# Optimization experiments

Measured on AMD Instinct MI355X. Metric: run time of the kernel, lower is better.

## Reference

```python
import jax, jax.numpy as jnp
import numpy as np

C = 4096
C8 = C // 8  # 512, must equal h*w
B, H, W = 32, 16, 32


def setup_inputs() -> dict:
    key = jax.random.key(0)
    ks = jax.random.split(key, 8)
    s = 0.02
    return {
        "x": jax.random.normal(ks[0], (B, C, H, W), dtype=jnp.float32),
        "Wq": jax.random.normal(ks[1], (C8, C), dtype=jnp.float32) * s,
        "bq": jax.random.normal(ks[2], (C8,), dtype=jnp.float32) * s,
        "Wk": jax.random.normal(ks[3], (C8, C), dtype=jnp.float32) * s,
        "bk": jax.random.normal(ks[4], (C8,), dtype=jnp.float32) * s,
        "Wv": jax.random.normal(ks[5], (C, C), dtype=jnp.float32) * s,
        "bv": jax.random.normal(ks[6], (C,), dtype=jnp.float32) * s,
        "gamma": jax.random.normal(ks[7], (1,), dtype=jnp.float32),
    }


def reference(x, Wq, bq, Wk, bk, Wv, bv, gamma):
    b, c, h, w = x.shape
    xf = x.reshape(b, c, h * w)               # (b, c, hw)
    # 1x1 conv == per-position linear over channels
    q = jnp.einsum("oc,bcl->bol", Wq, xf) + bq[None, :, None]   # (b, c8, hw)
    k = jnp.einsum("oc,bcl->bol", Wk, xf) + bk[None, :, None]   # (b, c8, hw)
    v = jnp.einsum("oc,bcl->bol", Wv, xf) + bv[None, :, None]   # (b, c, hw)
    # energy = bmm(Q, K^T): (b, c8, c8); no sqrt(d) scaling (faithful)
    energy = jnp.einsum("bol,bpl->bop", q, k)
    attn = jax.nn.softmax(energy, axis=-1)
    # out = bmm(V, attn^T): out[b,c,p] = sum_k V[b,c,k] * attn[b,p,k]
    out = jnp.einsum("bck,bpk->bcp", v, attn)  # requires hw == c8
    out = out.reshape(b, c, h, w)
    return gamma * out + x
```

## Files before the change

### kernel.cpp

```cpp
#include <hip/hip_runtime.h>


typedef _Float16 f16;
typedef _Float16 h8 __attribute__((ext_vector_type(8)));
typedef _Float16 h4 __attribute__((ext_vector_type(4)));
typedef float fx4 __attribute__((ext_vector_type(4)));

#define CC  4096
#define C8  512
#define HWD 512
#define NB  32

__device__ __forceinline__ h8 ldfragC(const char* s, int row, int cb) {
  const int b = ((row << 7) | cb) ^ ((row & 7) << 4);
  return *reinterpret_cast<const h8*>(s + b);
}

#define AS1C(p) ((const __attribute__((address_space(1))) unsigned int*)(p))
#define AS3(p)  ((__attribute__((address_space(3))) unsigned int*)(p))


#define STAGE_ALL(bufsel) { \
  char* la_ = smem + ((bufsel) << 16); \
  char* lb_ = la_ + 32768; \
  _Pragma("unroll") for (int q = 0; q < 4; ++q) { \
    __builtin_amdgcn_global_load_lds(AS1C(pA[q]), AS3(la_ + (q << 13) + w1024), 16, 0, 0); \
    __builtin_amdgcn_global_load_lds(AS1C(pB[q]), AS3(lb_ + (q << 13) + w1024), 16, 0, 0); \
    pA[q] += 128; pB[q] += 128; } }

#define STAGE2(bufsel, q) { \
  char* la_ = smem + ((bufsel) << 16); \
  char* lb_ = la_ + 32768; \
  __builtin_amdgcn_global_load_lds(AS1C(pA[q]), AS3(la_ + ((q) << 13) + w1024), 16, 0, 0); \
  __builtin_amdgcn_global_load_lds(AS1C(pB[q]), AS3(lb_ + ((q) << 13) + w1024), 16, 0, 0); \
  pA[q] += 128; pB[q] += 128; }

#define DSREADS_A(dst, hm, kh) \
  _Pragma("unroll") for (int f = 0; f < 4; ++f) \
    dst[f] = ldfragC(At, wr * 128 + (hm) * 64 + f * 16 + frow, (kh) * 64 + kq);

#define DSREADS_B(dst, kh) \
  _Pragma("unroll") for (int g = 0; g < 4; ++g) \
    dst[g] = ldfragC(Bt, wc * 64 + g * 16 + frow, (kh) * 64 + kq);

#define MMA16(hm, av, bv) \
  __builtin_amdgcn_s_setprio(1); \
  _Pragma("unroll") for (int f = 0; f < 4; ++f) \
  _Pragma("unroll") for (int g = 0; g < 4; ++g) \
    acc[(hm) * 4 + f][g] = __builtin_amdgcn_mfma_f32_16x16x32_f16( \
        av[f], bv[g], acc[(hm) * 4 + f][g], 0, 0, 0); \
  __builtin_amdgcn_s_setprio(0);

#define KTILE(cur, DOSTAGE) { \
  const bool dost_ = (DOSTAGE); \
  const char* At = smem + ((cur) << 16); \
  const char* Bt = At + 32768; \
  h8 a0[4], a1[4], b0[4], b1[4]; \
  asm volatile("s_waitcnt vmcnt(0)" ::: "memory"); \
  __builtin_amdgcn_s_barrier(); \
   \
  DSREADS_A(a0, 0, 0) DSREADS_B(b0, 0) \
  if (dost_) { STAGE2((cur) ^ 1, 0) STAGE2((cur) ^ 1, 1) } \
  __builtin_amdgcn_s_barrier(); \
  asm volatile("s_waitcnt lgkmcnt(0)"); \
  MMA16(0, a0, b0) \
  __builtin_amdgcn_s_barrier(); \
   \
  DSREADS_A(a1, 1, 0) \
  if (dost_) { STAGE2((cur) ^ 1, 2) STAGE2((cur) ^ 1, 3) } \
  __builtin_amdgcn_s_barrier(); \
  asm volatile("s_waitcnt lgkmcnt(0)"); \
  MMA16(1, a1, b0) \
  __builtin_amdgcn_s_barrier(); \
   \
  DSREADS_A(a0, 0, 1) DSREADS_B(b1, 1) \
  __builtin_amdgcn_s_barrier(); \
  asm volatile("s_waitcnt lgkmcnt(0)"); \
  MMA16(0, a0, b1) \
  __builtin_amdgcn_s_barrier(); \
   \
  DSREADS_A(a1, 1, 1) \
  __builtin_amdgcn_s_barrier(); \
  asm volatile("s_waitcnt lgkmcnt(0)"); \
  MMA16(1, a1, b1) \
  __builtin_amdgcn_s_barrier(); \
}

template<int EPI>
__global__ __launch_bounds__(512, 2) void gemm256(
    const f16* __restrict__ Ah, const f16* __restrict__ Bh,
    int lda, int ldb, long sAb, long sBb, long sCb, int ldc, int K,
    const float* __restrict__ bias, float* __restrict__ Cf, f16* __restrict__ Ch,
    const float* __restrict__ resid, const float* __restrict__ gam)
{
  extern __shared__ __align__(16) char smem[];
  const int F  = blockIdx.x;
  const int Vv = ((F & 7) << 7) | (F >> 3);
  const int bz = Vv >> 5;
  const int m0 = (Vv & 15) << 8;
  const int n0 = ((Vv >> 4) & 1) << 8;

  const int T = threadIdx.x;
  const int lane = T & 63;
  const int w = T >> 6;
  const int wr = w >> 2, wc = w & 3;
  const int frow = lane & 15;
  const int kq = (lane >> 4) << 4;
  const int w1024 = w << 10;

  const int rr = T >> 3;
  const int corig = ((T & 7) << 4) ^ ((rr & 7) << 4);
  const char* pA[4];
  const char* pB[4];
#pragma unroll
  for (int q = 0; q < 4; ++q) {
    pA[q] = (const char*)(Ah + bz * sAb + (long)(m0 + q * 64 + rr) * lda) + corig;
    pB[q] = (const char*)(Bh + bz * sBb + (long)(n0 + q * 64 + rr) * ldb) + corig;
  }

  fx4 acc[8][4] = {};
  const int nt = K >> 6;

  STAGE_ALL(0)
  for (int t = 0; t < nt; t += 2) {
    KTILE(0, t + 1 < nt)
    KTILE(1, t + 2 < nt)
  }

  const int cm = (lane >> 4) << 2;
  const int cn = lane & 15;
  const float g0 = (EPI == 3) ? gam[0] : 0.f;
#pragma unroll
  for (int fm = 0; fm < 8; ++fm) {
    const int gr0 = m0 + wr * 128 + fm * 16 + cm;
#pragma unroll
    for (int fn = 0; fn < 4; ++fn) {
      const int gc = n0 + wc * 64 + fn * 16 + cn;
#pragma unroll
      for (int j = 0; j < 4; ++j) {
        const long ci = bz * sCb + (long)(gr0 + j) * ldc + gc;
        if constexpr (EPI == 1) Ch[ci] = (f16)(acc[fm][fn][j] + bias[gr0 + j]);
        else                    Cf[ci] = g0 * acc[fm][fn][j] + resid[ci];
      }
    }
  }
}


#define TSTG(p, off, ldB) { \
  _Pragma("unroll") for (int q = 0; q < 4; ++q) \
    __builtin_amdgcn_global_load_lds(AS1C((p) + (long)q * 32 * (ldB)), \
        AS3(smt + (off) + (q << 12) + (T << 4)), 16, 0, 0); \
  (p) += 128; }

template<int EPI>
__global__ __launch_bounds__(256) void gemm_tri(
    const f16* __restrict__ Ah, const f16* __restrict__ Al,
    const f16* __restrict__ Bh, const f16* __restrict__ Bl,
    int K, int lda, int ldb, long sAb, long sBb, long sCb, int ldc,
    const float* __restrict__ bias,
    float* __restrict__ Cf, f16* __restrict__ Ch, f16* __restrict__ Cl)
{
  __shared__ __align__(16) char smt[65536];

  const int bz = blockIdx.z;
  const int m0 = blockIdx.y * 128, n0 = blockIdx.x * 128;
  const int T = threadIdx.x;
  const int lane = T & 63;
  const int wid  = T >> 6;
  const int wr = wid >> 1, wc = wid & 1;
  const int frow = lane & 15;
  const int kq = (lane >> 4) << 4;

  const int rr = T >> 3;
  const int cor = ((T & 7) << 4) ^ ((rr & 7) << 4);
  const long ldaB = (long)lda * 2, ldbB = (long)ldb * 2;
  const char* pAh = (const char*)(Ah + (long)bz * sAb + (long)(m0 + rr) * lda) + cor;
  const char* pAl = (const char*)(Al + (long)bz * sAb + (long)(m0 + rr) * lda) + cor;
  const char* pBh = (const char*)(Bh + (long)bz * sBb + (long)(n0 + rr) * ldb) + cor;
  const char* pBl = (const char*)(Bl + (long)bz * sBb + (long)(n0 + rr) * ldb) + cor;

  const char* sAh = smt;
  const char* sBh = smt + 16384;
  const char* sAl = smt + 32768;
  const char* sBl = smt + 49152;

  fx4 acc[4][4] = {};

  for (int k0 = 0; k0 < K; k0 += 64) {
    TSTG(pAh, 0, ldaB)
    TSTG(pBh, 16384, ldbB)
    TSTG(pAl, 32768, ldaB)
    TSTG(pBl, 49152, ldbB)
    asm volatile("s_waitcnt vmcnt(0)" ::: "memory");
    __syncthreads();
#pragma unroll
    for (int ks = 0; ks < 2; ++ks) {
      const int kb = ks * 64 + kq;
      h8 aH[4], bH[4], aL[4], bL[4];
#pragma unroll
      for (int f = 0; f < 4; ++f) {
        aH[f] = ldfragC(sAh, wr * 64 + f * 16 + frow, kb);
        bH[f] = ldfragC(sBh, wc * 64 + f * 16 + frow, kb);
        aL[f] = ldfragC(sAl, wr * 64 + f * 16 + frow, kb);
        bL[f] = ldfragC(sBl, wc * 64 + f * 16 + frow, kb);
      }
#pragma unroll
      for (int fm = 0; fm < 4; ++fm)
#pragma unroll
        for (int fn = 0; fn < 4; ++fn) {
          acc[fm][fn] = __builtin_amdgcn_mfma_f32_16x16x32_f16(aH[fm], bH[fn], acc[fm][fn], 0, 0, 0);
          acc[fm][fn] = __builtin_amdgcn_mfma_f32_16x16x32_f16(aH[fm], bL[fn], acc[fm][fn], 0, 0, 0);
          acc[fm][fn] = __builtin_amdgcn_mfma_f32_16x16x32_f16(aL[fm], bH[fn], acc[fm][fn], 0, 0, 0);
        }
    }
    __syncthreads();
  }

  const int cm = (lane >> 4) * 4;
  const int cn = lane & 15;
#pragma unroll
  for (int fm = 0; fm < 4; ++fm) {
    const int gr0 = m0 + wr * 64 + fm * 16 + cm;
#pragma unroll
    for (int fn = 0; fn < 4; ++fn) {
      const int gc = n0 + wc * 64 + fn * 16 + cn;
#pragma unroll
      for (int j = 0; j < 4; ++j) {
        const int gr = gr0 + j;
        const long ci = (long)bz * sCb + (long)gr * ldc + gc;
        float v = acc[fm][fn][j];
        if constexpr (EPI == 0) {
          v += bias[gr];
          const f16 h = (f16)v;
          Ch[ci] = h;
          Cl[ci] = (f16)(v - (float)h);
        } else {
          Cf[ci] = v;
        }
      }
    }
  }
}

__global__ void transpose_split_k(const float* __restrict__ x, f16* __restrict__ xh, f16* __restrict__ xl) {
  __shared__ float t[32][33];
  const int l0 = blockIdx.x * 32, c0 = blockIdx.y * 32;
  const long bi = (long)blockIdx.z * CC * HWD;
  const long bo = (long)blockIdx.z * HWD * CC;
  const int tx = threadIdx.x, ty = threadIdx.y;
#pragma unroll
  for (int i = 0; i < 32; i += 8)
    t[ty + i][tx] = x[bi + (long)(c0 + ty + i) * HWD + l0 + tx];
  __syncthreads();
#pragma unroll
  for (int i = 0; i < 32; i += 8) {
    const float v = t[tx][ty + i];
    const f16 h = (f16)v;
    const long o = bo + (long)(l0 + ty + i) * CC + c0 + tx;
    xh[o] = h;
    xl[o] = (f16)(v - (float)h);
  }
}

template<bool HASLO>
__global__ void split_k(const float* __restrict__ in, f16* __restrict__ hi, f16* __restrict__ lo, long n) {
  const long i = ((long)blockIdx.x * blockDim.x + threadIdx.x) * 4;
  if (i >= n) return;
  const float4 v = *reinterpret_cast<const float4*>(in + i);
  const float vv[4] = {v.x, v.y, v.z, v.w};
  h4 h, l;
#pragma unroll
  for (int j = 0; j < 4; ++j) {
    const f16 hh = (f16)vv[j];
    h[j] = hh;
    l[j] = (f16)(vv[j] - (float)hh);
  }
  *reinterpret_cast<h4*>(hi + i) = h;
  if constexpr (HASLO) *reinterpret_cast<h4*>(lo + i) = l;
}

__global__ __launch_bounds__(256) void softmax_k(const float* __restrict__ E, f16* __restrict__ attn) {
  const int lane = threadIdx.x & 63;
  const int wid  = threadIdx.x >> 6;
  const long row = (long)blockIdx.x * 4 + wid;
  const float* e = E + row * 512;
  const float4 a = *reinterpret_cast<const float4*>(e + lane * 8);
  const float4 b = *reinterpret_cast<const float4*>(e + lane * 8 + 4);
  float vv[8] = {a.x, a.y, a.z, a.w, b.x, b.y, b.z, b.w};
  float m = vv[0];
#pragma unroll
  for (int i = 1; i < 8; ++i) m = fmaxf(m, vv[i]);
#pragma unroll
  for (int s = 32; s > 0; s >>= 1) m = fmaxf(m, __shfl_xor(m, s));
  float sum = 0.f;
  float ex[8];
#pragma unroll
  for (int i = 0; i < 8; ++i) { ex[i] = __expf(vv[i] - m); sum += ex[i]; }
#pragma unroll
  for (int s = 32; s > 0; s >>= 1) sum += __shfl_xor(sum, s);
  const float inv = 1.f / sum;
  h8 o;
#pragma unroll
  for (int i = 0; i < 8; ++i) o[i] = (f16)(ex[i] * inv);
  *reinterpret_cast<h8*>(attn + row * 512 + lane * 8) = o;
}

extern "C" void kernel_launch(void* const* d_in, const int* in_sizes, int n_in,
                              void* d_out, int out_size, void* d_ws, size_t ws_size,
                              hipStream_t stream) {
  const float* x  = (const float*)d_in[0];
  const float* Wq = (const float*)d_in[1];
  const float* bq = (const float*)d_in[2];
  const float* Wk = (const float*)d_in[3];
  const float* bk = (const float*)d_in[4];
  const float* Wv = (const float*)d_in[5];
  const float* bv = (const float*)d_in[6];
  const float* gm = (const float*)d_in[7];
  float* out = (float*)d_out;

  const size_t szXT = (size_t)NB * HWD * CC;
  const size_t szQK = (size_t)NB * C8 * HWD;
  const size_t szW  = (size_t)C8 * CC;
  const size_t szWv = (size_t)CC * CC;
  const size_t needBytes = (2 * szXT + 4 * szQK + 4 * szW + szWv) * sizeof(f16);
  if (ws_size < needBytes) return;

  f16* xT_h = (f16*)d_ws;
  f16* xT_l = xT_h + szXT;
  f16* v16  = xT_l;
  f16* q_h  = xT_h + 2 * szXT;
  f16* q_l  = q_h + szQK;
  f16* k_h  = q_l + szQK;
  f16* k_l  = k_h + szQK;
  f16* wq_h = k_l + szQK;
  f16* wq_l = wq_h + szW;
  f16* wk_h = wq_l + szW;
  f16* wk_l = wk_h + szW;
  f16* attn = wq_h;
  f16* wv_h = wk_l + szW;
  float* E  = (float*)wv_h;

  split_k<true ><<<dim3((C8 * CC) / 1024), 256, 0, stream>>>(Wq, wq_h, wq_l, (long)C8 * CC);
  split_k<true ><<<dim3((C8 * CC) / 1024), 256, 0, stream>>>(Wk, wk_h, wk_l, (long)C8 * CC);
  split_k<false><<<dim3((CC * CC) / 1024), 256, 0, stream>>>(Wv, wv_h, nullptr, (long)CC * CC);
  transpose_split_k<<<dim3(HWD / 32, CC / 32, NB), dim3(32, 8), 0, stream>>>(x, xT_h, xT_l);
  gemm_tri<0><<<dim3(4, 4, NB), 256, 0, stream>>>(wq_h, wq_l, xT_h, xT_l, CC, CC, CC,
      0L, (long)HWD * CC, (long)C8 * HWD, HWD, bq, nullptr, q_h, q_l);
  gemm_tri<0><<<dim3(4, 4, NB), 256, 0, stream>>>(wk_h, wk_l, xT_h, xT_l, CC, CC, CC,
      0L, (long)HWD * CC, (long)C8 * HWD, HWD, bk, nullptr, k_h, k_l);
  gemm256<1><<<dim3(1024), 512, 131072, stream>>>(wv_h, xT_h, CC, CC,
      0L, (long)HWD * CC, (long)CC * HWD, HWD, CC, bv, nullptr, v16, nullptr, nullptr);
  gemm_tri<2><<<dim3(4, 4, NB), 256, 0, stream>>>(q_h, q_l, k_h, k_l, HWD, HWD, HWD,
      (long)C8 * HWD, (long)C8 * HWD, (long)C8 * C8, C8, nullptr, E, nullptr, nullptr);
  softmax_k<<<dim3(NB * C8 / 4), 256, 0, stream>>>(E, attn);
  gemm256<3><<<dim3(1024), 512, 131072, stream>>>(v16, attn, HWD, HWD,
      (long)CC * HWD, (long)C8 * HWD, (long)CC * HWD, HWD, C8, nullptr, out, nullptr, x, gm);
}
```

Baseline: 1.268 ms.

## Use partial vmcnt waits in gemm256 staging and vectorize transpose stores

Splits gemm256's global-to-LDS staging into A and B pieces, issues six loads in the first half of each k-tile and two in the second, and replaces the full vmcnt(0) waits with partial vmcnt counts. Each tile then waits only for the loads it needs, so the next tile's prefetch can stay in flight during the MFMAs. The transpose kernel also moves to a 16x16 block and writes fp16 hi/lo pairs as 2-element vector stores. The risk is that a wrong vmcnt count lets a wave read LDS before its data has landed.

```diff
diff --git a/kernel.cpp b/kernel.cpp
--- a/kernel.cpp
+++ b/kernel.cpp
@@ -4,6 +4,7 @@
 typedef _Float16 f16;
 typedef _Float16 h8 __attribute__((ext_vector_type(8)));
 typedef _Float16 h4 __attribute__((ext_vector_type(4)));
+typedef _Float16 h2 __attribute__((ext_vector_type(2)));
 typedef float fx4 __attribute__((ext_vector_type(4)));
 
 #define CC  4096
@@ -20,20 +21,17 @@
 #define AS3(p)  ((__attribute__((address_space(3))) unsigned int*)(p))
 
 
-#define STAGE_ALL(bufsel) { \
-  char* la_ = smem + ((bufsel) << 16); \
-  char* lb_ = la_ + 32768; \
-  _Pragma("unroll") for (int q = 0; q < 4; ++q) { \
-    __builtin_amdgcn_global_load_lds(AS1C(pA[q]), AS3(la_ + (q << 13) + w1024), 16, 0, 0); \
-    __builtin_amdgcn_global_load_lds(AS1C(pB[q]), AS3(lb_ + (q << 13) + w1024), 16, 0, 0); \
-    pA[q] += 128; pB[q] += 128; } }
-
-#define STAGE2(bufsel, q) { \
-  char* la_ = smem + ((bufsel) << 16); \
-  char* lb_ = la_ + 32768; \
-  __builtin_amdgcn_global_load_lds(AS1C(pA[q]), AS3(la_ + ((q) << 13) + w1024), 16, 0, 0); \
-  __builtin_amdgcn_global_load_lds(AS1C(pB[q]), AS3(lb_ + ((q) << 13) + w1024), 16, 0, 0); \
-  pA[q] += 128; pB[q] += 128; }
+#define STGA(bufsel, q) { \
+  __builtin_amdgcn_global_load_lds(AS1C(pA[q]), \
+      AS3(smem + ((bufsel) << 16) + ((q) << 13) + w1024), 16, 0, 0); \
+  pA[q] += 128; }
+#define STGB(bufsel, q) { \
+  __builtin_amdgcn_global_load_lds(AS1C(pB[q]), \
+      AS3(smem + ((bufsel) << 16) + 32768 + ((q) << 13) + w1024), 16, 0, 0); \
+  pB[q] += 128; }
+
+#define STG6(bufsel) { STGA(bufsel,0) STGA(bufsel,2) STGB(bufsel,0) STGB(bufsel,1) STGB(bufsel,2) STGB(bufsel,3) }
+#define STG2(bufsel) { STGA(bufsel,1) STGA(bufsel,3) }
 
 #define DSREADS_A(dst, hm, kh) \
   _Pragma("unroll") for (int f = 0; f < 4; ++f) \
@@ -51,23 +49,24 @@
         av[f], bv[g], acc[(hm) * 4 + f][g], 0, 0, 0); \
   __builtin_amdgcn_s_setprio(0);
 
-#define KTILE(cur, DOSTAGE) { \
-  const bool dost_ = (DOSTAGE); \
+#define KTILE(cur, dost, last) { \
   const char* At = smem + ((cur) << 16); \
   const char* Bt = At + 32768; \
   h8 a0[4], a1[4], b0[4], b1[4]; \
-  asm volatile("s_waitcnt vmcnt(0)" ::: "memory"); \
+  asm volatile("s_waitcnt vmcnt(2)" ::: "memory"); \
   __builtin_amdgcn_s_barrier(); \
    \
   DSREADS_A(a0, 0, 0) DSREADS_B(b0, 0) \
-  if (dost_) { STAGE2((cur) ^ 1, 0) STAGE2((cur) ^ 1, 1) } \
+  if (dost) STG6((cur) ^ 1) \
   __builtin_amdgcn_s_barrier(); \
   asm volatile("s_waitcnt lgkmcnt(0)"); \
   MMA16(0, a0, b0) \
+  if (last) { asm volatile("s_waitcnt vmcnt(0)" ::: "memory"); } \
+  else      { asm volatile("s_waitcnt vmcnt(6)" ::: "memory"); } \
   __builtin_amdgcn_s_barrier(); \
    \
   DSREADS_A(a1, 1, 0) \
-  if (dost_) { STAGE2((cur) ^ 1, 2) STAGE2((cur) ^ 1, 3) } \
+  if (dost) STG2((cur) ^ 1) \
   __builtin_amdgcn_s_barrier(); \
   asm volatile("s_waitcnt lgkmcnt(0)"); \
   MMA16(1, a1, b0) \
@@ -121,10 +120,10 @@
   fx4 acc[8][4] = {};
   const int nt = K >> 6;
 
-  STAGE_ALL(0)
+  STG6(0) STG2(0)
   for (int t = 0; t < nt; t += 2) {
-    KTILE(0, t + 1 < nt)
-    KTILE(1, t + 2 < nt)
+    KTILE(0, 1, 0)
+    KTILE(1, t + 2 < nt, t + 2 == nt)
   }
 
   const int cm = (lane >> 4) << 2;
@@ -145,7 +144,6 @@
     }
   }
 }
-
 
 #define TSTG(p, off, ldB) { \
   _Pragma("unroll") for (int q = 0; q < 4; ++q) \
@@ -250,16 +248,21 @@
   const long bo = (long)blockIdx.z * HWD * CC;
   const int tx = threadIdx.x, ty = threadIdx.y;
 #pragma unroll
-  for (int i = 0; i < 32; i += 8)
-    t[ty + i][tx] = x[bi + (long)(c0 + ty + i) * HWD + l0 + tx];
+  for (int i = 0; i < 2; ++i)
+#pragma unroll
+    for (int j = 0; j < 2; ++j)
+      t[ty + 16 * i][tx + 16 * j] = x[bi + (long)(c0 + ty + 16 * i) * HWD + l0 + tx + 16 * j];
   __syncthreads();
 #pragma unroll
-  for (int i = 0; i < 32; i += 8) {
-    const float v = t[tx][ty + i];
-    const f16 h = (f16)v;
-    const long o = bo + (long)(l0 + ty + i) * CC + c0 + tx;
-    xh[o] = h;
-    xl[o] = (f16)(v - (float)h);
+  for (int i = 0; i < 2; ++i) {
+    const int l = ty + 16 * i;
+    const float v0 = t[2 * tx][l], v1 = t[2 * tx + 1][l];
+    const f16 h0 = (f16)v0, h1 = (f16)v1;
+    const long o = bo + (long)(l0 + l) * CC + c0 + 2 * tx;
+    h2 hh; hh[0] = h0; hh[1] = h1;
+    h2 ll; ll[0] = (f16)(v0 - (float)h0); ll[1] = (f16)(v1 - (float)h1);
+    *reinterpret_cast<h2*>(xh + o) = hh;
+    *reinterpret_cast<h2*>(xl + o) = ll;
   }
 }
 
@@ -344,7 +347,7 @@
   split_k<true ><<<dim3((C8 * CC) / 1024), 256, 0, stream>>>(Wq, wq_h, wq_l, (long)C8 * CC);
   split_k<true ><<<dim3((C8 * CC) / 1024), 256, 0, stream>>>(Wk, wk_h, wk_l, (long)C8 * CC);
   split_k<false><<<dim3((CC * CC) / 1024), 256, 0, stream>>>(Wv, wv_h, nullptr, (long)CC * CC);
-  transpose_split_k<<<dim3(HWD / 32, CC / 32, NB), dim3(32, 8), 0, stream>>>(x, xT_h, xT_l);
+  transpose_split_k<<<dim3(HWD / 32, CC / 32, NB), dim3(16, 16), 0, stream>>>(x, xT_h, xT_l);
   gemm_tri<0><<<dim3(4, 4, NB), 256, 0, stream>>>(wq_h, wq_l, xT_h, xT_l, CC, CC, CC,
       0L, (long)HWD * CC, (long)C8 * HWD, HWD, bq, nullptr, q_h, q_l);
   gemm_tri<0><<<dim3(4, 4, NB), 256, 0, stream>>>(wk_h, wk_l, xT_h, xT_l, CC, CC, CC,
```

New measurement: 2.329 ms. 1.84x slower.
